# Optimization experiments

Hardware: AMD Instinct MI355X
Metric: run time of the kernel (lower is better)

The kernel has to match this reference:

```python
import jax, jax.numpy as jnp
import numpy as np

D_MODEL = 512; D_K = 64; D_V = 64; H = 8; NX = 6; D_FF = 2048; VOCAB = 37000
BN_EPS = 1e-5


def setup_inputs() -> dict:
    key = jax.random.key(0)
    ks = jax.random.split(key, 20)
    B, S, SE = 4, 512, 512
    g = lambda k, shape, sc: jax.random.normal(k, shape, jnp.float32) * sc
    return {
        'output': jax.random.randint(ks[0], (B, S), 0, VOCAB),
        'encoder_result': g(ks[1], (B, SE, D_MODEL), 1.0),
        'emb': g(ks[2], (VOCAB, D_MODEL), 0.02),
        'Wq1': g(ks[3], (NX, H, D_MODEL, D_K), 0.04),
        'Wk1': g(ks[4], (NX, H, D_MODEL, D_K), 0.04),
        'Wv1': g(ks[5], (NX, H, D_MODEL, D_V), 0.04),
        'Wo1': g(ks[6], (NX, H * D_V, D_MODEL), 0.04),
        'Wq2': g(ks[7], (NX, H, D_MODEL, D_K), 0.04),
        'Wk2': g(ks[8], (NX, H, D_MODEL, D_K), 0.04),
        'Wv2': g(ks[9], (NX, H, D_MODEL, D_V), 0.04),
        'Wo2': g(ks[10], (NX, H * D_V, D_MODEL), 0.04),
        'gamma': jnp.ones((NX, 3, D_MODEL), jnp.float32),
        'beta': jnp.zeros((NX, 3, D_MODEL), jnp.float32),
        'W1': g(ks[11], (NX, D_MODEL, D_FF), 0.04),
        'b1': jnp.zeros((NX, D_FF), jnp.float32),
        'W2': g(ks[12], (NX, D_FF, D_MODEL), 0.02),
        'b2': jnp.zeros((NX, D_MODEL), jnp.float32),
        'Wout': g(ks[13], (D_MODEL, VOCAB), 0.04),
        'bout': jnp.zeros((VOCAB,), jnp.float32),
    }


def _mha(xq, xkv, Wq, Wk, Wv, Wo, causal):
    # Wq/Wk/Wv: [H, D, dk]; batched form of the original per-head Linear loop
    Q = jnp.einsum('bsd,hde->bhse', xq, Wq)
    K = jnp.einsum('btd,hde->bhte', xkv, Wk)
    V = jnp.einsum('btd,hde->bhte', xkv, Wv)
    scores = jnp.einsum('bhse,bhte->bhst', Q, K) / jnp.sqrt(jnp.float32(D_K))
    if causal:
        s = xq.shape[1]
        m = jnp.triu(jnp.ones((s, s), bool), 1)  # future positions
        scores = jnp.where(m, -jnp.inf, scores)
    A = jax.nn.softmax(scores, axis=-1)
    out = jnp.einsum('bhst,bhte->bhse', A, V)  # [B,H,S,dv]
    out = out.transpose(0, 2, 1, 3).reshape(xq.shape[0], xq.shape[1], H * D_V)
    return out @ Wo


def _bn(x, g, b):
    # BatchNorm1d(d_model) in training mode on [B, D, S] == per-channel over (B, S)
    mu = x.mean(axis=(0, 1))
    var = x.var(axis=(0, 1))  # biased, matches torch BN normalization
    return (x - mu) * jax.lax.rsqrt(var + BN_EPS) * g + b


def reference(output, encoder_result, emb, Wq1, Wk1, Wv1, Wo1, Wq2, Wk2, Wv2, Wo2,
              gamma, beta, W1, b1, W2, b2, Wout, bout):
    x = emb[output] * np.sqrt(D_K).astype(np.float32)  # note: sqrt(d_k), as in source
    for i in range(NX):
        x = _bn(x + _mha(x, x, Wq1[i], Wk1[i], Wv1[i], Wo1[i], True), gamma[i, 0], beta[i, 0])
        x = _bn(x + _mha(x, encoder_result, Wq2[i], Wk2[i], Wv2[i], Wo2[i], False), gamma[i, 1], beta[i, 1])
        ff = jax.nn.relu(x @ W1[i] + b1[i]) @ W2[i] + b2[i]
        x = _bn(x + ff, gamma[i, 2], beta[i, 2])
    return jax.nn.softmax(x @ Wout + bout, axis=-1)
```

## Files before the change

kernel.cpp:

```cpp
#include <hip/hip_runtime.h>
#include <math.h>

static constexpr int Bc   = 4;
static constexpr int Sc   = 512;
static constexpr int Dc   = 512;
static constexpr int Hc   = 8;
static constexpr int DKc  = 64;
static constexpr int NXc  = 6;
static constexpr int DFFc = 2048;
static constexpr int Vc   = 37000;
static constexpr int Mc   = Bc * Sc;
static constexpr float BN_EPS = 1e-5f;

#define NEG_INF (-1e30f)

using bf16x8 = __attribute__((ext_vector_type(8))) short;
using f32x4  = __attribute__((ext_vector_type(4))) float;

__device__ inline unsigned short f2bf(float f) {
  union { float f; unsigned u; } v; v.f = f;
  unsigned r = v.u + 0x7FFFu + ((v.u >> 16) & 1u);
  return (unsigned short)(r >> 16);
}

__device__ inline bf16x8 cvt8(float4 a, float4 b) {
  union { bf16x8 v; unsigned short s[8]; } u;
  u.s[0] = f2bf(a.x); u.s[1] = f2bf(a.y); u.s[2] = f2bf(a.z); u.s[3] = f2bf(a.w);
  u.s[4] = f2bf(b.x); u.s[5] = f2bf(b.y); u.s[6] = f2bf(b.z); u.s[7] = f2bf(b.w);
  return u.v;
}

__device__ inline bf16x8 pack8(const float* f) {
  union { bf16x8 v; unsigned short s[8]; } u;
#pragma unroll
  for (int i = 0; i < 8; i++) u.s[i] = f2bf(f[i]);
  return u.v;
}

__global__ void embed_k(const int* __restrict__ idx, const float* __restrict__ emb,
                        float* __restrict__ x) {
  int i = blockIdx.x * blockDim.x + threadIdx.x;
  if (i >= Mc * Dc) return;
  int r = i >> 9;
  int d = i & 511;
  x[i] = emb[(long)idx[r] * Dc + d] * 8.0f;
}

__global__ __launch_bounds__(256) void gemm_nn_mfma(
    const float* __restrict__ A, const float* __restrict__ B0,
    const float* __restrict__ bias, float* __restrict__ C,
    int M, int N, int K, long aB, long bB, long cB,
    float alpha, int relu)
{
  int z = blockIdx.z;
  const float* Ap = A  + (long)z * aB;
  const float* Bp = B0 + (long)z * bB;
  C += (long)z * cB;

  __shared__ unsigned short sA[128 * 32];
  __shared__ unsigned short sB[128 * 32];

  int tid  = threadIdx.x;
  int lane = tid & 63;
  int wave = tid >> 6;
  int row0 = blockIdx.x * 128, col0 = blockIdx.y * 128;

  int ar = tid >> 1, akh = (tid & 1) * 16;
  int bcc = tid & 127, bkh = (tid >> 7) * 16;
  bool bok = (col0 + bcc < N);

  float4 ra[4];
  float  rbs[16];

  auto load_tiles = [&](int k0) {
#pragma unroll
    for (int p = 0; p < 4; p++)
      ra[p] = *(const float4*)(Ap + (long)(row0 + ar) * K + k0 + akh + p * 4);
#pragma unroll
    for (int i = 0; i < 16; i++)
      rbs[i] = bok ? Bp[(long)(k0 + bkh + i) * N + col0 + bcc] : 0.f;
  };

  f32x4 zero4 = {0.f, 0.f, 0.f, 0.f};
  f32x4 acc[4][4];
#pragma unroll
  for (int i = 0; i < 4; i++)
#pragma unroll
    for (int j = 0; j < 4; j++) acc[i][j] = zero4;

  int m0 = (wave >> 1) * 64, n0 = (wave & 1) * 64;
  int fr = lane & 15;

  int aU0 = (ar >> 4) * 64 + ((akh >> 3) + 0) * 16 + (ar & 15);
  int aU1 = (ar >> 4) * 64 + ((akh >> 3) + 1) * 16 + (ar & 15);
  int bU0 = (bcc >> 4) * 64 + ((bkh >> 3) + 0) * 16 + (bcc & 15);
  int bU1 = (bcc >> 4) * 64 + ((bkh >> 3) + 1) * 16 + (bcc & 15);

  load_tiles(0);
  for (int k0 = 0; ; ) {
    __syncthreads();
    *(bf16x8*)&sA[aU0 * 8] = cvt8(ra[0], ra[1]);
    *(bf16x8*)&sA[aU1 * 8] = cvt8(ra[2], ra[3]);
    *(bf16x8*)&sB[bU0 * 8] = pack8(&rbs[0]);
    *(bf16x8*)&sB[bU1 * 8] = pack8(&rbs[8]);
    __syncthreads();

    int kn = k0 + 32;
    bool more = kn < K;
    if (more) load_tiles(kn);

    bf16x8 af[4], bfr[4];
#pragma unroll
    for (int i = 0; i < 4; i++) {
      af[i]  = *(const bf16x8*)&sA[(((m0 >> 4) + i) * 64 + lane) * 8];
      bfr[i] = *(const bf16x8*)&sB[(((n0 >> 4) + i) * 64 + lane) * 8];
    }
#pragma unroll
    for (int mi = 0; mi < 4; mi++)
#pragma unroll
      for (int ni = 0; ni < 4; ni++)
        acc[mi][ni] = __builtin_amdgcn_mfma_f32_16x16x32_bf16(af[mi], bfr[ni], acc[mi][ni], 0, 0, 0);

    if (!more) break;
    k0 = kn;
  }

  int rg = (lane >> 4) << 2;
#pragma unroll
  for (int ni = 0; ni < 4; ni++) {
    int col = col0 + n0 + ni * 16 + fr;
    if (col < N) {
      float bv = bias ? bias[col] : 0.f;
#pragma unroll
      for (int mi = 0; mi < 4; mi++) {
        int r0 = row0 + m0 + mi * 16 + rg;
#pragma unroll
        for (int j = 0; j < 4; j++) {
          float o = acc[mi][ni][j] * alpha + bv;
          if (relu) o = fmaxf(o, 0.f);
          C[(long)(r0 + j) * N + col] = o;
        }
      }
    }
  }
}

__global__ __launch_bounds__(256) void gemm64(
    const float* __restrict__ A, const float* __restrict__ A2,
    const float* __restrict__ B0, const float* __restrict__ B1, const float* __restrict__ B2,
    const float* __restrict__ bias, float* __restrict__ C,
    int N, int K, long aB, long bB, long cB, int mode, int relu)
{
  int z = blockIdx.z;
  const float* Ap;
  const float* Bp;
  float* Cp;
  int ldc;
  if (mode == 2) {
    int t = z >> 5, zz = z & 31;
    Ap = (t == 0 ? A : A2) + (long)(zz >> 3) * aB;
    Bp = (t == 0 ? B0 : (t == 1 ? B1 : B2)) + (long)(zz & 7) * bB;
    Cp = C + (long)z * cB; ldc = N;
  } else if (mode == 3) {
    Ap = A + (long)z * aB; Bp = B0 + (long)z * bB;
    Cp = C + (long)(z >> 3) * ((long)Sc * Dc) + (long)(z & 7) * 64; ldc = Dc;
  } else {
    Ap = A + (long)z * aB; Bp = B0 + (long)z * bB;
    Cp = C + (long)z * cB; ldc = N;
  }

  __shared__ unsigned short sA[64 * 64];
  __shared__ unsigned short sB[64 * 64];

  int tid = threadIdx.x, lane = tid & 63, wave = tid >> 6;
  int row0 = blockIdx.x * 64, col0 = blockIdx.y * 64;

  int ar = tid >> 2, akq = (tid & 3) * 16;
  int bcc = lane, bkq = wave * 16;

  float4 ra[4];
  float  rbs[16];
  auto load_tiles = [&](int k0) {
#pragma unroll
    for (int p = 0; p < 4; p++)
      ra[p] = *(const float4*)(Ap + (long)(row0 + ar) * K + k0 + akq + p * 4);
#pragma unroll
    for (int i = 0; i < 16; i++)
      rbs[i] = Bp[(long)(k0 + bkq + i) * N + col0 + bcc];
  };

  int aU0 = ((ar >> 4) * 2 + (akq >> 5)) * 64 + ((akq >> 3) & 3) * 16 + (ar & 15);
  int aU1 = ((ar >> 4) * 2 + ((akq + 8) >> 5)) * 64 + (((akq + 8) >> 3) & 3) * 16 + (ar & 15);
  int bU0 = ((bcc >> 4) * 2 + (bkq >> 5)) * 64 + ((bkq >> 3) & 3) * 16 + (bcc & 15);
  int bU1 = ((bcc >> 4) * 2 + ((bkq + 8) >> 5)) * 64 + (((bkq + 8) >> 3) & 3) * 16 + (bcc & 15);

  f32x4 zero4 = {0.f, 0.f, 0.f, 0.f};
  f32x4 acc[2][2];
  acc[0][0] = zero4; acc[0][1] = zero4; acc[1][0] = zero4; acc[1][1] = zero4;

  int m0 = (wave >> 1) * 32, n0 = (wave & 1) * 32;
  int fr = lane & 15;

  load_tiles(0);
  for (int k0 = 0; ; ) {
    __syncthreads();
    *(bf16x8*)&sA[aU0 * 8] = cvt8(ra[0], ra[1]);
    *(bf16x8*)&sA[aU1 * 8] = cvt8(ra[2], ra[3]);
    *(bf16x8*)&sB[bU0 * 8] = pack8(&rbs[0]);
    *(bf16x8*)&sB[bU1 * 8] = pack8(&rbs[8]);
    __syncthreads();

    int kn = k0 + 64;
    bool more = kn < K;
    if (more) load_tiles(kn);

    bf16x8 af[2][2], bf[2][2];
#pragma unroll
    for (int i = 0; i < 2; i++)
#pragma unroll
      for (int kk = 0; kk < 2; kk++) {
        af[i][kk] = *(const bf16x8*)&sA[((((m0 >> 4) + i) * 2 + kk) * 64 + lane) * 8];
        bf[i][kk] = *(const bf16x8*)&sB[((((n0 >> 4) + i) * 2 + kk) * 64 + lane) * 8];
      }
#pragma unroll
    for (int kk = 0; kk < 2; kk++)
#pragma unroll
      for (int mi = 0; mi < 2; mi++)
#pragma unroll
        for (int ni = 0; ni < 2; ni++)
          acc[mi][ni] = __builtin_amdgcn_mfma_f32_16x16x32_bf16(af[mi][kk], bf[ni][kk], acc[mi][ni], 0, 0, 0);

    if (!more) break;
    k0 = kn;
  }

  int rg = (lane >> 4) << 2;
#pragma unroll
  for (int ni = 0; ni < 2; ni++) {
    int col = col0 + n0 + ni * 16 + fr;
    float bv = bias ? bias[col] : 0.f;
#pragma unroll
    for (int mi = 0; mi < 2; mi++) {
      int r0 = row0 + m0 + mi * 16 + rg;
#pragma unroll
      for (int j = 0; j < 4; j++) {
        float o = acc[mi][ni][j] + bv;
        if (relu) o = fmaxf(o, 0.f);
        Cp[(long)(r0 + j) * ldc + col] = o;
      }
    }
  }
}

__global__ __launch_bounds__(256) void gemm_nt_mfma(
    const float* __restrict__ A, const float* __restrict__ Bm, float* __restrict__ C,
    long aB, long bB, long cB, float alpha, int causal)
{
  if (causal && blockIdx.y > blockIdx.x) return;
  int z = blockIdx.z;
  const float* Ap = A  + (long)z * aB;
  const float* Bp = Bm + (long)z * bB;
  float* Cp = C + (long)z * cB;

  int tid = threadIdx.x, lane = tid & 63, wave = tid >> 6;
  int m0 = blockIdx.x * 128 + (wave >> 1) * 64;
  int n0 = blockIdx.y * 128 + (wave & 1) * 64;
  int fr = lane & 15, fk = (lane >> 4) * 8;

  bf16x8 af[4][2];
#pragma unroll
  for (int mi = 0; mi < 4; mi++) {
    const float* p = Ap + (long)(m0 + mi * 16 + fr) * DKc + fk;
    af[mi][0] = cvt8(*(const float4*)p,        *(const float4*)(p + 4));
    af[mi][1] = cvt8(*(const float4*)(p + 32), *(const float4*)(p + 36));
  }

  f32x4 zero4 = {0.f, 0.f, 0.f, 0.f};
  f32x4 acc[4][4];
#pragma unroll
  for (int i = 0; i < 4; i++)
#pragma unroll
    for (int j = 0; j < 4; j++) acc[i][j] = zero4;

#pragma unroll
  for (int ni = 0; ni < 4; ni++) {
    const float* q = Bp + (long)(n0 + ni * 16 + fr) * DKc + fk;
    bf16x8 b0 = cvt8(*(const float4*)q,        *(const float4*)(q + 4));
    bf16x8 b1 = cvt8(*(const float4*)(q + 32), *(const float4*)(q + 36));
#pragma unroll
    for (int mi = 0; mi < 4; mi++) {
      acc[mi][ni] = __builtin_amdgcn_mfma_f32_16x16x32_bf16(af[mi][0], b0, acc[mi][ni], 0, 0, 0);
      acc[mi][ni] = __builtin_amdgcn_mfma_f32_16x16x32_bf16(af[mi][1], b1, acc[mi][ni], 0, 0, 0);
    }
  }

  int rg = (lane >> 4) << 2;
#pragma unroll
  for (int ni = 0; ni < 4; ni++) {
    int col = n0 + ni * 16 + fr;
#pragma unroll
    for (int mi = 0; mi < 4; mi++) {
      int r0 = m0 + mi * 16 + rg;
#pragma unroll
      for (int j = 0; j < 4; j++)
        Cp[(long)(r0 + j) * Sc + col] = acc[mi][ni][j] * alpha;
    }
  }
}

__global__ __launch_bounds__(256) void attn_softmax(float* __restrict__ sc, int causal) {
  int row = blockIdx.x;
  int s = row & (Sc - 1);
  float* p = sc + (long)row * Sc;
  int t0 = threadIdx.x, t1 = threadIdx.x + 256;
  int limit = causal ? (s + 1) : Sc;

  float v0 = (t0 < limit) ? p[t0] : NEG_INF;
  float v1 = (t1 < limit) ? p[t1] : NEG_INF;
  float mx = fmaxf(v0, v1);
  __shared__ float sm[4], sm2[4];
#pragma unroll
  for (int o = 32; o > 0; o >>= 1) mx = fmaxf(mx, __shfl_down(mx, o, 64));
  if ((threadIdx.x & 63) == 0) sm[threadIdx.x >> 6] = mx;
  __syncthreads();
  mx = fmaxf(fmaxf(sm[0], sm[1]), fmaxf(sm[2], sm[3]));

  float e0 = (t0 < limit) ? __expf(v0 - mx) : 0.f;
  float e1 = (t1 < limit) ? __expf(v1 - mx) : 0.f;
  float sum = e0 + e1;
#pragma unroll
  for (int o = 32; o > 0; o >>= 1) sum += __shfl_down(sum, o, 64);
  if ((threadIdx.x & 63) == 0) sm2[threadIdx.x >> 6] = sum;
  __syncthreads();
  sum = sm2[0] + sm2[1] + sm2[2] + sm2[3];
  float inv = 1.f / sum;
  p[t0] = e0 * inv;
  p[t1] = e1 * inv;
}

__global__ __launch_bounds__(256) void add_stats(
    float* __restrict__ x, const float* __restrict__ y, float* __restrict__ part)
{
  int blk = blockIdx.x;
  int c = threadIdx.x * 2;
  int r0 = blk * 16;
  float s0 = 0.f, s1 = 0.f, q0 = 0.f, q1 = 0.f;
#pragma unroll 4
  for (int r = r0; r < r0 + 16; r++) {
    long off = (long)r * Dc + c;
    float2 v = *(const float2*)&x[off];
    float2 w = *(const float2*)&y[off];
    v.x += w.x; v.y += w.y;
    *(float2*)&x[off] = v;
    s0 += v.x; q0 += v.x * v.x;
    s1 += v.y; q1 += v.y * v.y;
  }
  part[(long)c * 128 + blk] = s0;
  part[(long)(c + 1) * 128 + blk] = s1;
  part[Dc * 128 + (long)c * 128 + blk] = q0;
  part[Dc * 128 + (long)(c + 1) * 128 + blk] = q1;
}

__global__ __launch_bounds__(256) void bn_finalize(
    const float* __restrict__ part, const float* __restrict__ g,
    const float* __restrict__ b, float* __restrict__ scale, float* __restrict__ shift)
{
  int c = blockIdx.x * 256 + threadIdx.x;
  if (c >= Dc) return;
  const float* ps = part + (long)c * 128;
  const float* pq = part + Dc * 128 + (long)c * 128;
  float s = 0.f, q = 0.f;
#pragma unroll 8
  for (int i = 0; i < 128; i++) { s += ps[i]; q += pq[i]; }
  float mu  = s * (1.f / Mc);
  float var = q * (1.f / Mc) - mu * mu;
  float sc = g[c] * rsqrtf(var + BN_EPS);
  scale[c] = sc;
  shift[c] = b[c] - mu * sc;
}

__global__ void bn_apply(float* __restrict__ x, const float* __restrict__ scale,
                         const float* __restrict__ shift) {
  int i = blockIdx.x * blockDim.x + threadIdx.x;
  if (i >= Mc * Dc) return;
  int c = i & 511;
  x[i] = x[i] * scale[c] + shift[c];
}

static constexpr int VT = 37;
__global__ __launch_bounds__(1024) void vocab_softmax(float* __restrict__ out) {
  long row = blockIdx.x;
  float* p = out + row * (long)Vc;
  float v[VT];
  float mx = NEG_INF;
#pragma unroll
  for (int j = 0; j < VT; j++) {
    int c = threadIdx.x + j * 1024;
    v[j] = (c < Vc) ? p[c] : NEG_INF;
    mx = fmaxf(mx, v[j]);
  }
  __shared__ float sm[16], sm2[16];
#pragma unroll
  for (int o = 32; o > 0; o >>= 1) mx = fmaxf(mx, __shfl_down(mx, o, 64));
  if ((threadIdx.x & 63) == 0) sm[threadIdx.x >> 6] = mx;
  __syncthreads();
  float m2 = sm[0];
#pragma unroll
  for (int i = 1; i < 16; i++) m2 = fmaxf(m2, sm[i]);
  mx = m2;

  float sum = 0.f;
#pragma unroll
  for (int j = 0; j < VT; j++) {
    int c = threadIdx.x + j * 1024;
    float e = (c < Vc) ? __expf(v[j] - mx) : 0.f;
    v[j] = e; sum += e;
  }
#pragma unroll
  for (int o = 32; o > 0; o >>= 1) sum += __shfl_down(sum, o, 64);
  if ((threadIdx.x & 63) == 0) sm2[threadIdx.x >> 6] = sum;
  __syncthreads();
  float s2 = 0.f;
#pragma unroll
  for (int i = 0; i < 16; i++) s2 += sm2[i];
  float inv = 1.f / s2;
#pragma unroll
  for (int j = 0; j < VT; j++) {
    int c = threadIdx.x + j * 1024;
    if (c < Vc) p[c] = v[j] * inv;
  }
}

extern "C" void kernel_launch(void* const* d_in, const int* in_sizes, int n_in,
                              void* d_out, int out_size, void* d_ws, size_t ws_size,
                              hipStream_t stream) {
  const int*   idx   = (const int*)d_in[0];
  const float* enc   = (const float*)d_in[1];
  const float* emb   = (const float*)d_in[2];
  const float* Wq1   = (const float*)d_in[3];
  const float* Wk1   = (const float*)d_in[4];
  const float* Wv1   = (const float*)d_in[5];
  const float* Wo1   = (const float*)d_in[6];
  const float* Wq2   = (const float*)d_in[7];
  const float* Wk2   = (const float*)d_in[8];
  const float* Wv2   = (const float*)d_in[9];
  const float* Wo2   = (const float*)d_in[10];
  const float* gamma = (const float*)d_in[11];
  const float* beta  = (const float*)d_in[12];
  const float* W1    = (const float*)d_in[13];
  const float* b1    = (const float*)d_in[14];
  const float* W2    = (const float*)d_in[15];
  const float* b2    = (const float*)d_in[16];
  const float* Wout  = (const float*)d_in[17];
  const float* bout  = (const float*)d_in[18];
  float* out = (float*)d_out;

  float* ws = (float*)d_ws;
  const long MD = (long)Mc * Dc;
  float* x      = ws;
  float* t0     = x  + MD;
  float* Q      = t0 + MD;
  float* Kb     = Q  + MD;
  float* Vb     = Kb + MD;
  float* cc     = Vb + MD;
  float* ff1    = cc + MD;
  float* scores = ff1 + (long)Mc * DFFc;
  float* scalep = scores + (long)Bc * Hc * Sc * Sc;
  float* shiftp = scalep + Dc;
  float* part   = shiftp + Dc;

  const int n1 = Mc * Dc;
  const int eb = (n1 + 255) / 256;
  const long sSD  = (long)Sc * Dc;
  const long sDK  = (long)Dc * DKc;
  const long sSK  = (long)Sc * DKc;
  const long sSS  = (long)Sc * Sc;

  embed_k<<<eb, 256, 0, stream>>>(idx, emb, x);

  for (int l = 0; l < NXc; l++) {
    {
      const float* wq = Wq1 + (long)l * Hc * Dc * DKc;
      const float* wk = Wk1 + (long)l * Hc * Dc * DKc;
      const float* wv = Wv1 + (long)l * Hc * Dc * DKc;
      const float* wo = Wo1 + (long)l * Dc * Dc;
      gemm64<<<dim3(Sc / 64, 1, 96), 256, 0, stream>>>(
          x, x, wq, wk, wv, nullptr, Q, DKc, Dc, sSD, sDK, sSK, 2, 0);
      gemm_nt_mfma<<<dim3(4, 4, Bc * Hc), 256, 0, stream>>>(
          Q, Kb, scores, sSK, sSK, sSS, 0.125f, 1);
      attn_softmax<<<Bc * Hc * Sc, 256, 0, stream>>>(scores, 1);
      gemm64<<<dim3(Sc / 64, 1, Bc * Hc), 256, 0, stream>>>(
          scores, nullptr, Vb, nullptr, nullptr, nullptr, cc, DKc, Sc, sSS, sSK, 0, 3, 0);
      gemm64<<<dim3(Mc / 64, Dc / 64, 1), 256, 0, stream>>>(
          cc, nullptr, wo, nullptr, nullptr, nullptr, t0, Dc, Dc, 0, 0, 0, 0, 0);
      add_stats<<<128, 256, 0, stream>>>(x, t0, part);
      bn_finalize<<<2, 256, 0, stream>>>(part, gamma + (long)(l * 3 + 0) * Dc, beta + (long)(l * 3 + 0) * Dc, scalep, shiftp);
      bn_apply<<<eb, 256, 0, stream>>>(x, scalep, shiftp);
    }
    {
      const float* wq = Wq2 + (long)l * Hc * Dc * DKc;
      const float* wk = Wk2 + (long)l * Hc * Dc * DKc;
      const float* wv = Wv2 + (long)l * Hc * Dc * DKc;
      const float* wo = Wo2 + (long)l * Dc * Dc;
      gemm64<<<dim3(Sc / 64, 1, 96), 256, 0, stream>>>(
          x, enc, wq, wk, wv, nullptr, Q, DKc, Dc, sSD, sDK, sSK, 2, 0);
      gemm_nt_mfma<<<dim3(4, 4, Bc * Hc), 256, 0, stream>>>(
          Q, Kb, scores, sSK, sSK, sSS, 0.125f, 0);
      attn_softmax<<<Bc * Hc * Sc, 256, 0, stream>>>(scores, 0);
      gemm64<<<dim3(Sc / 64, 1, Bc * Hc), 256, 0, stream>>>(
          scores, nullptr, Vb, nullptr, nullptr, nullptr, cc, DKc, Sc, sSS, sSK, 0, 3, 0);
      gemm64<<<dim3(Mc / 64, Dc / 64, 1), 256, 0, stream>>>(
          cc, nullptr, wo, nullptr, nullptr, nullptr, t0, Dc, Dc, 0, 0, 0, 0, 0);
      add_stats<<<128, 256, 0, stream>>>(x, t0, part);
      bn_finalize<<<2, 256, 0, stream>>>(part, gamma + (long)(l * 3 + 1) * Dc, beta + (long)(l * 3 + 1) * Dc, scalep, shiftp);
      bn_apply<<<eb, 256, 0, stream>>>(x, scalep, shiftp);
    }
    {
      gemm_nn_mfma<<<dim3(Mc / 128, DFFc / 128, 1), 256, 0, stream>>>(
          x, W1 + (long)l * Dc * DFFc, b1 + (long)l * DFFc, ff1,
          Mc, DFFc, Dc, 0, 0, 0, 1.f, 1);
      gemm64<<<dim3(Mc / 64, Dc / 64, 1), 256, 0, stream>>>(
          ff1, nullptr, W2 + (long)l * DFFc * Dc, nullptr, nullptr, b2 + (long)l * Dc, t0,
          Dc, DFFc, 0, 0, 0, 0, 0);
      add_stats<<<128, 256, 0, stream>>>(x, t0, part);
      bn_finalize<<<2, 256, 0, stream>>>(part, gamma + (long)(l * 3 + 2) * Dc, beta + (long)(l * 3 + 2) * Dc, scalep, shiftp);
      bn_apply<<<eb, 256, 0, stream>>>(x, scalep, shiftp);
    }
  }

  gemm_nn_mfma<<<dim3(Mc / 128, (Vc + 127) / 128, 1), 256, 0, stream>>>(
      x, Wout, bout, out, Mc, Vc, Dc, 0, 0, 0, 1.f, 0);
  vocab_softmax<<<Mc, 1024, 0, stream>>>(out);
}
```

Before: 2.420 ms.

## Convert activations and weights to bf16 with transposed layouts and direct-to-LDS loads

Adds a weight conversion kernel that transposes all projection, FFN and output weights into bf16 K-major layouts, either all up front or per layer depending on workspace size. Activations (x, encoder output, Q/K/V, attention probabilities, FFN hidden) are now stored as bf16 alongside fp32 x. The GEMMs are rewritten to load bf16 tiles straight into LDS with global_load_lds, and the large GEMMs use a 128x128 kernel with an LDS-staged, vectorised epilogue. The aim is less global memory traffic and no in-kernel fp32-to-bf16 conversion, at the price of an extra weight-conversion pass on every call and lower precision of stored intermediates.

```diff
diff --git a/kernel.cpp b/kernel.cpp
--- a/kernel.cpp
+++ b/kernel.cpp
@@ -14,252 +14,300 @@
 
 #define NEG_INF (-1e30f)
 
+typedef unsigned short u16;
 using bf16x8 = __attribute__((ext_vector_type(8))) short;
+using us8    = __attribute__((ext_vector_type(8))) unsigned short;
 using f32x4  = __attribute__((ext_vector_type(4))) float;
 
-__device__ inline unsigned short f2bf(float f) {
+__device__ inline u16 f2bf(float f) {
   union { float f; unsigned u; } v; v.f = f;
   unsigned r = v.u + 0x7FFFu + ((v.u >> 16) & 1u);
-  return (unsigned short)(r >> 16);
-}
-
-__device__ inline bf16x8 cvt8(float4 a, float4 b) {
-  union { bf16x8 v; unsigned short s[8]; } u;
-  u.s[0] = f2bf(a.x); u.s[1] = f2bf(a.y); u.s[2] = f2bf(a.z); u.s[3] = f2bf(a.w);
-  u.s[4] = f2bf(b.x); u.s[5] = f2bf(b.y); u.s[6] = f2bf(b.z); u.s[7] = f2bf(b.w);
-  return u.v;
-}
-
-__device__ inline bf16x8 pack8(const float* f) {
-  union { bf16x8 v; unsigned short s[8]; } u;
-#pragma unroll
-  for (int i = 0; i < 8; i++) u.s[i] = f2bf(f[i]);
-  return u.v;
+  return (u16)(r >> 16);
+}
+
+__device__ inline void gload16(const void* g, void* l) {
+  __builtin_amdgcn_global_load_lds(
+      (const __attribute__((address_space(1))) unsigned int*)g,
+      (__attribute__((address_space(3))) unsigned int*)l, 16, 0, 0);
 }
 
 __global__ void embed_k(const int* __restrict__ idx, const float* __restrict__ emb,
-                        float* __restrict__ x) {
+                        float* __restrict__ x, u16* __restrict__ xh) {
   int i = blockIdx.x * blockDim.x + threadIdx.x;
   if (i >= Mc * Dc) return;
-  int r = i >> 9;
-  int d = i & 511;
-  x[i] = emb[(long)idx[r] * Dc + d] * 8.0f;
-}
-
-__global__ __launch_bounds__(256) void gemm_nn_mfma(
-    const float* __restrict__ A, const float* __restrict__ B0,
-    const float* __restrict__ bias, float* __restrict__ C,
-    int M, int N, int K, long aB, long bB, long cB,
-    float alpha, int relu)
+  int r = i >> 9, d = i & 511;
+  float v = emb[(long)idx[r] * Dc + d] * 8.0f;
+  x[i] = v;
+  xh[i] = f2bf(v);
+}
+
+__global__ void cvt_bf16(const float* __restrict__ in, u16* __restrict__ out, int n4) {
+  int i = blockIdx.x * blockDim.x + threadIdx.x;
+  if (i >= n4) return;
+  float4 v = ((const float4*)in)[i];
+  unsigned a = (unsigned)f2bf(v.x) | ((unsigned)f2bf(v.y) << 16);
+  unsigned b = (unsigned)f2bf(v.z) | ((unsigned)f2bf(v.w) << 16);
+  uint2 w; w.x = a; w.y = b;
+  ((uint2*)out)[i] = w;
+}
+
+__device__ void wtile(const float* src, int ldin, int cval, u16* dst, int ldout) {
+  __shared__ u16 ls[64][65];
+  int tx = threadIdx.x & 63, ty = threadIdx.x >> 6;
+#pragma unroll
+  for (int p = 0; p < 16; p++) {
+    int r = p * 4 + ty;
+    float v = (tx < cval) ? src[(long)r * ldin + tx] : 0.f;
+    ls[tx][r] = f2bf(v);
+  }
+  __syncthreads();
+#pragma unroll
+  for (int p = 0; p < 16; p++) {
+    int oc = p * 4 + ty;
+    dst[(long)oc * ldout + tx] = ls[oc][tx];
+  }
+}
+
+__global__ __launch_bounds__(256) void wconv(
+    const float* q1, const float* k1, const float* v1, const float* o1,
+    const float* q2, const float* k2, const float* v2, const float* o2,
+    const float* w1, const float* w2, const float* wout,
+    u16* Wb, u16* WoutT, int nl, int l0)
 {
-  int z = blockIdx.z;
-  const float* Ap = A  + (long)z * aB;
-  const float* Bp = B0 + (long)z * bB;
-  C += (long)z * cB;
-
-  __shared__ unsigned short sA[128 * 32];
-  __shared__ unsigned short sB[128 * 32];
-
-  int tid  = threadIdx.x;
-  int lane = tid & 63;
-  int wave = tid >> 6;
+  long HT = (long)nl * 262144;
+  int u = blockIdx.x;
+  int layerBlocks = nl * 1024;
+  if (u < layerBlocks) {
+    int lslot = u >> 10;
+    int l = l0 + lslot;
+    int t = u & 1023;
+    if (t < 384) {
+      int ten = t >> 6, w = t & 63, h = w >> 3, rt = w & 7;
+      const float* base = (ten == 0) ? q1 : (ten == 1) ? k1 : (ten == 2) ? v1
+                         : (ten == 3) ? q2 : (ten == 4) ? k2 : v2;
+      const float* src = base + ((long)l * 8 + h) * 32768 + (long)rt * 64 * 64;
+      u16* dst = Wb + (long)ten * HT + (long)lslot * 262144 + (long)h * 32768 + rt * 64;
+      wtile(src, 64, 64, dst, 512);
+    } else if (t < 512) {
+      int v_ = t - 384, o = v_ >> 6, w = v_ & 63, rt = w >> 3, ct = w & 7;
+      const float* src = (o ? o2 : o1) + (long)l * 262144 + (long)rt * 64 * 512 + ct * 64;
+      u16* dst = Wb + (long)(6 + o) * HT + (long)lslot * 262144 + (long)ct * 64 * 512 + rt * 64;
+      wtile(src, 512, 64, dst, 512);
+    } else if (t < 768) {
+      int v_ = t - 512, rt = v_ >> 5, ct = v_ & 31;
+      const float* src = w1 + (long)l * 1048576 + (long)rt * 64 * 2048 + ct * 64;
+      u16* dst = Wb + 8 * HT + (long)lslot * 1048576 + (long)ct * 64 * 512 + rt * 64;
+      wtile(src, 2048, 64, dst, 512);
+    } else {
+      int v_ = t - 768, rt = v_ >> 3, ct = v_ & 7;
+      const float* src = w2 + (long)l * 1048576 + (long)rt * 64 * 512 + ct * 64;
+      u16* dst = Wb + 12 * HT + (long)lslot * 1048576 + (long)ct * 64 * 2048 + rt * 64;
+      wtile(src, 512, 64, dst, 2048);
+    }
+  } else {
+    int v_ = u - layerBlocks;
+    int rt = v_ & 7, ct = v_ >> 3;
+    int c0 = ct * 64;
+    int cv = Vc - c0; cv = cv < 0 ? 0 : (cv > 64 ? 64 : cv);
+    const float* src = wout + (long)rt * 64 * Vc + c0;
+    u16* dst = WoutT + (long)c0 * 512 + rt * 64;
+    wtile(src, Vc, cv, dst, 512);
+  }
+}
+
+__global__ __launch_bounds__(256) void gemm128(
+    const u16* __restrict__ A, const u16* __restrict__ Bt,
+    const float* __restrict__ bias, void* __restrict__ Cv,
+    int N, int K, int obf, int relu)
+{
+  __shared__ u16 smem[2 * 128 * 64];
+  u16* sA = smem;
+  u16* sB = smem + 128 * 64;
+
+  int tid = threadIdx.x, lane = tid & 63, wave = tid >> 6;
   int row0 = blockIdx.x * 128, col0 = blockIdx.y * 128;
-
-  int ar = tid >> 1, akh = (tid & 1) * 16;
-  int bcc = tid & 127, bkh = (tid >> 7) * 16;
-  bool bok = (col0 + bcc < N);
-
-  float4 ra[4];
-  float  rbs[16];
-
-  auto load_tiles = [&](int k0) {
-#pragma unroll
-    for (int p = 0; p < 4; p++)
-      ra[p] = *(const float4*)(Ap + (long)(row0 + ar) * K + k0 + akh + p * 4);
-#pragma unroll
-    for (int i = 0; i < 16; i++)
-      rbs[i] = bok ? Bp[(long)(k0 + bkh + i) * N + col0 + bcc] : 0.f;
-  };
-
-  f32x4 zero4 = {0.f, 0.f, 0.f, 0.f};
+  int frs = lane & 15, kq = lane >> 4;
+
+  const u16* pA[4]; const u16* pB[4]; u16* lA[4]; u16* lB[4];
+#pragma unroll
+  for (int i = 0; i < 4; i++) {
+    int idx = wave * 4 + i, mi = idx >> 1, kgh = idx & 1;
+    pA[i] = A  + (long)(row0 + mi * 16 + frs) * K + kgh * 32 + kq * 8;
+    pB[i] = Bt + (long)(col0 + mi * 16 + frs) * K + kgh * 32 + kq * 8;
+    lA[i] = sA + (mi * 2 + kgh) * 512;
+    lB[i] = sB + (mi * 2 + kgh) * 512;
+  }
+
   f32x4 acc[4][4];
 #pragma unroll
   for (int i = 0; i < 4; i++)
 #pragma unroll
-    for (int j = 0; j < 4; j++) acc[i][j] = zero4;
+    for (int j = 0; j < 4; j++) acc[i][j] = (f32x4){0.f, 0.f, 0.f, 0.f};
 
   int m0 = (wave >> 1) * 64, n0 = (wave & 1) * 64;
-  int fr = lane & 15;
-
-  int aU0 = (ar >> 4) * 64 + ((akh >> 3) + 0) * 16 + (ar & 15);
-  int aU1 = (ar >> 4) * 64 + ((akh >> 3) + 1) * 16 + (ar & 15);
-  int bU0 = (bcc >> 4) * 64 + ((bkh >> 3) + 0) * 16 + (bcc & 15);
-  int bU1 = (bcc >> 4) * 64 + ((bkh >> 3) + 1) * 16 + (bcc & 15);
-
-  load_tiles(0);
-  for (int k0 = 0; ; ) {
+
+  for (int kt = 0; kt < K; kt += 64) {
+#pragma unroll
+    for (int i = 0; i < 4; i++) { gload16(pA[i], lA[i]); pA[i] += 64; }
+#pragma unroll
+    for (int i = 0; i < 4; i++) { gload16(pB[i], lB[i]); pB[i] += 64; }
     __syncthreads();
-    *(bf16x8*)&sA[aU0 * 8] = cvt8(ra[0], ra[1]);
-    *(bf16x8*)&sA[aU1 * 8] = cvt8(ra[2], ra[3]);
-    *(bf16x8*)&sB[bU0 * 8] = pack8(&rbs[0]);
-    *(bf16x8*)&sB[bU1 * 8] = pack8(&rbs[8]);
+#pragma unroll
+    for (int ks = 0; ks < 2; ks++) {
+      bf16x8 af[4], bf[4];
+#pragma unroll
+      for (int i = 0; i < 4; i++) {
+        af[i] = *(const bf16x8*)&sA[(((m0 >> 4) + i) * 128 + ks * 64 + lane) * 8];
+        bf[i] = *(const bf16x8*)&sB[(((n0 >> 4) + i) * 128 + ks * 64 + lane) * 8];
+      }
+#pragma unroll
+      for (int mi = 0; mi < 4; mi++)
+#pragma unroll
+        for (int ni = 0; ni < 4; ni++)
+          acc[mi][ni] = __builtin_amdgcn_mfma_f32_16x16x32_bf16(af[mi], bf[ni], acc[mi][ni], 0, 0, 0);
+    }
     __syncthreads();
-
-    int kn = k0 + 32;
-    bool more = kn < K;
-    if (more) load_tiles(kn);
-
-    bf16x8 af[4], bfr[4];
-#pragma unroll
-    for (int i = 0; i < 4; i++) {
-      af[i]  = *(const bf16x8*)&sA[(((m0 >> 4) + i) * 64 + lane) * 8];
-      bfr[i] = *(const bf16x8*)&sB[(((n0 >> 4) + i) * 64 + lane) * 8];
-    }
-#pragma unroll
-    for (int mi = 0; mi < 4; mi++)
-#pragma unroll
-      for (int ni = 0; ni < 4; ni++)
-        acc[mi][ni] = __builtin_amdgcn_mfma_f32_16x16x32_bf16(af[mi], bfr[ni], acc[mi][ni], 0, 0, 0);
-
-    if (!more) break;
-    k0 = kn;
-  }
-
-  int rg = (lane >> 4) << 2;
-#pragma unroll
-  for (int ni = 0; ni < 4; ni++) {
-    int col = col0 + n0 + ni * 16 + fr;
-    if (col < N) {
-      float bv = bias ? bias[col] : 0.f;
-#pragma unroll
-      for (int mi = 0; mi < 4; mi++) {
-        int r0 = row0 + m0 + mi * 16 + rg;
-#pragma unroll
-        for (int j = 0; j < 4; j++) {
-          float o = acc[mi][ni][j] * alpha + bv;
-          if (relu) o = fmaxf(o, 0.f);
-          C[(long)(r0 + j) * N + col] = o;
-        }
-      }
-    }
-  }
-}
-
-__global__ __launch_bounds__(256) void gemm64(
-    const float* __restrict__ A, const float* __restrict__ A2,
-    const float* __restrict__ B0, const float* __restrict__ B1, const float* __restrict__ B2,
-    const float* __restrict__ bias, float* __restrict__ C,
-    int N, int K, long aB, long bB, long cB, int mode, int relu)
-{
-  int z = blockIdx.z;
-  const float* Ap;
-  const float* Bp;
-  float* Cp;
-  int ldc;
-  if (mode == 2) {
-    int t = z >> 5, zz = z & 31;
-    Ap = (t == 0 ? A : A2) + (long)(zz >> 3) * aB;
-    Bp = (t == 0 ? B0 : (t == 1 ? B1 : B2)) + (long)(zz & 7) * bB;
-    Cp = C + (long)z * cB; ldc = N;
-  } else if (mode == 3) {
-    Ap = A + (long)z * aB; Bp = B0 + (long)z * bB;
-    Cp = C + (long)(z >> 3) * ((long)Sc * Dc) + (long)(z & 7) * 64; ldc = Dc;
-  } else {
-    Ap = A + (long)z * aB; Bp = B0 + (long)z * bB;
-    Cp = C + (long)z * cB; ldc = N;
-  }
-
-  __shared__ unsigned short sA[64 * 64];
-  __shared__ unsigned short sB[64 * 64];
-
-  int tid = threadIdx.x, lane = tid & 63, wave = tid >> 6;
-  int row0 = blockIdx.x * 64, col0 = blockIdx.y * 64;
-
-  int ar = tid >> 2, akq = (tid & 3) * 16;
-  int bcc = lane, bkq = wave * 16;
-
-  float4 ra[4];
-  float  rbs[16];
-  auto load_tiles = [&](int k0) {
-#pragma unroll
-    for (int p = 0; p < 4; p++)
-      ra[p] = *(const float4*)(Ap + (long)(row0 + ar) * K + k0 + akq + p * 4);
-#pragma unroll
-    for (int i = 0; i < 16; i++)
-      rbs[i] = Bp[(long)(k0 + bkq + i) * N + col0 + bcc];
-  };
-
-  int aU0 = ((ar >> 4) * 2 + (akq >> 5)) * 64 + ((akq >> 3) & 3) * 16 + (ar & 15);
-  int aU1 = ((ar >> 4) * 2 + ((akq + 8) >> 5)) * 64 + (((akq + 8) >> 3) & 3) * 16 + (ar & 15);
-  int bU0 = ((bcc >> 4) * 2 + (bkq >> 5)) * 64 + ((bkq >> 3) & 3) * 16 + (bcc & 15);
-  int bU1 = ((bcc >> 4) * 2 + ((bkq + 8) >> 5)) * 64 + (((bkq + 8) >> 3) & 3) * 16 + (bcc & 15);
-
-  f32x4 zero4 = {0.f, 0.f, 0.f, 0.f};
-  f32x4 acc[2][2];
-  acc[0][0] = zero4; acc[0][1] = zero4; acc[1][0] = zero4; acc[1][1] = zero4;
-
-  int m0 = (wave >> 1) * 32, n0 = (wave & 1) * 32;
-  int fr = lane & 15;
-
-  load_tiles(0);
-  for (int k0 = 0; ; ) {
-    __syncthreads();
-    *(bf16x8*)&sA[aU0 * 8] = cvt8(ra[0], ra[1]);
-    *(bf16x8*)&sA[aU1 * 8] = cvt8(ra[2], ra[3]);
-    *(bf16x8*)&sB[bU0 * 8] = pack8(&rbs[0]);
-    *(bf16x8*)&sB[bU1 * 8] = pack8(&rbs[8]);
-    __syncthreads();
-
-    int kn = k0 + 64;
-    bool more = kn < K;
-    if (more) load_tiles(kn);
-
-    bf16x8 af[2][2], bf[2][2];
-#pragma unroll
-    for (int i = 0; i < 2; i++)
-#pragma unroll
-      for (int kk = 0; kk < 2; kk++) {
-        af[i][kk] = *(const bf16x8*)&sA[((((m0 >> 4) + i) * 2 + kk) * 64 + lane) * 8];
-        bf[i][kk] = *(const bf16x8*)&sB[((((n0 >> 4) + i) * 2 + kk) * 64 + lane) * 8];
-      }
-#pragma unroll
-    for (int kk = 0; kk < 2; kk++)
-#pragma unroll
-      for (int mi = 0; mi < 2; mi++)
-#pragma unroll
-        for (int ni = 0; ni < 2; ni++)
-          acc[mi][ni] = __builtin_amdgcn_mfma_f32_16x16x32_bf16(af[mi][kk], bf[ni][kk], acc[mi][ni], 0, 0, 0);
-
-    if (!more) break;
-    k0 = kn;
-  }
-
-  int rg = (lane >> 4) << 2;
-#pragma unroll
-  for (int ni = 0; ni < 2; ni++) {
-    int col = col0 + n0 + ni * 16 + fr;
-    float bv = bias ? bias[col] : 0.f;
-#pragma unroll
-    for (int mi = 0; mi < 2; mi++) {
-      int r0 = row0 + m0 + mi * 16 + rg;
+  }
+
+  float* scr = (float*)smem + wave * (16 * 68);
+  int rg = kq * 4;
+  u16* Cus = (u16*)Cv; float* Cf = (float*)Cv;
+#pragma unroll
+  for (int mi = 0; mi < 4; mi++) {
+#pragma unroll
+    for (int ni = 0; ni < 4; ni++) {
+      int colg = col0 + n0 + ni * 16 + frs;
+      float bv = bias ? ((colg < N) ? bias[colg] : 0.f) : 0.f;
 #pragma unroll
       for (int j = 0; j < 4; j++) {
         float o = acc[mi][ni][j] + bv;
         if (relu) o = fmaxf(o, 0.f);
-        Cp[(long)(r0 + j) * ldc + col] = o;
+        scr[(rg + j) * 68 + ni * 16 + frs] = o;
       }
     }
+    int rbase = row0 + m0 + mi * 16;
+    if (obf) {
+#pragma unroll
+      for (int p = 0; p < 2; p++) {
+        int rowl = p * 8 + (lane >> 3), c8 = (lane & 7) * 8;
+        float4 v0 = *(const float4*)&scr[rowl * 68 + c8];
+        float4 v1 = *(const float4*)&scr[rowl * 68 + c8 + 4];
+        union { us8 v; u16 s[8]; } w;
+        w.s[0] = f2bf(v0.x); w.s[1] = f2bf(v0.y); w.s[2] = f2bf(v0.z); w.s[3] = f2bf(v0.w);
+        w.s[4] = f2bf(v1.x); w.s[5] = f2bf(v1.y); w.s[6] = f2bf(v1.z); w.s[7] = f2bf(v1.w);
+        *(us8*)&Cus[(long)(rbase + rowl) * N + col0 + n0 + c8] = w.v;
+      }
+    } else {
+#pragma unroll
+      for (int p = 0; p < 4; p++) {
+        int rowl = p * 4 + kq, c4 = frs * 4;
+        int colg = col0 + n0 + c4;
+        float4 v = *(const float4*)&scr[rowl * 68 + c4];
+        if (colg < N)
+          *(float4*)&Cf[(long)(rbase + rowl) * N + colg] = v;
+      }
+    }
+  }
+}
+
+__global__ __launch_bounds__(256) void gemm64(
+    const u16* __restrict__ A, const u16* __restrict__ A2,
+    const u16* __restrict__ Bt, const float* __restrict__ bias, void* __restrict__ Cv,
+    int N, int K, int lda, long aB, long btB, long cB, long tQK, int mode, int obf)
+{
+  int z = blockIdx.z;
+  const u16* Ap; const u16* Btp; long coff; int ldc;
+  if (mode == 1) {
+    int t = z >> 5, zz = z & 31;
+    Ap = (t == 0 ? A : A2) + (long)(zz >> 3) * aB;
+    Btp = Bt + (long)t * tQK + (long)(zz & 7) * btB;
+    coff = (long)z * cB; ldc = N;
+  } else if (mode == 2) {
+    Ap = A + (long)(z & 7) * aB;
+    Btp = Bt + (long)(z >> 3) * btB;
+    coff = (long)z * cB; ldc = N;
+  } else if (mode == 3) {
+    Ap = A + (long)z * aB;
+    Btp = Bt + (long)z * btB;
+    coff = (long)(z >> 3) * (512 * 512) + (long)(z & 7) * 64; ldc = 512;
+  } else {
+    Ap = A + (long)z * aB;
+    Btp = Bt + (long)z * btB;
+    coff = (long)z * cB; ldc = N;
+  }
+
+  __shared__ u16 smem[2 * 64 * 64];
+  u16* sA = smem; u16* sB = smem + 4096;
+
+  int tid = threadIdx.x, lane = tid & 63, wave = tid >> 6;
+  int row0 = blockIdx.x * 64, col0 = blockIdx.y * 64;
+  int frs = lane & 15, kq = lane >> 4;
+
+  const u16* pA[2]; const u16* pB[2]; u16* lA[2]; u16* lB[2];
+#pragma unroll
+  for (int i = 0; i < 2; i++) {
+    pA[i] = Ap  + (long)(row0 + wave * 16 + frs) * lda + i * 32 + kq * 8;
+    pB[i] = Btp + (long)(col0 + wave * 16 + frs) * K   + i * 32 + kq * 8;
+    lA[i] = sA + (wave * 2 + i) * 512;
+    lB[i] = sB + (wave * 2 + i) * 512;
+  }
+
+  f32x4 acc[2][2];
+  acc[0][0] = acc[0][1] = acc[1][0] = acc[1][1] = (f32x4){0.f, 0.f, 0.f, 0.f};
+  int m0 = (wave >> 1) * 32, n0 = (wave & 1) * 32;
+
+  for (int kt = 0; kt < K; kt += 64) {
+#pragma unroll
+    for (int i = 0; i < 2; i++) {
+      gload16(pA[i], lA[i]); pA[i] += 64;
+      gload16(pB[i], lB[i]); pB[i] += 64;
+    }
+    __syncthreads();
+    bf16x8 af[2][2], bf[2][2];
+#pragma unroll
+    for (int i = 0; i < 2; i++)
+#pragma unroll
+      for (int ks = 0; ks < 2; ks++) {
+        af[i][ks] = *(const bf16x8*)&sA[(((m0 >> 4) + i) * 128 + ks * 64 + lane) * 8];
+        bf[i][ks] = *(const bf16x8*)&sB[(((n0 >> 4) + i) * 128 + ks * 64 + lane) * 8];
+      }
+#pragma unroll
+    for (int ks = 0; ks < 2; ks++)
+#pragma unroll
+      for (int mi = 0; mi < 2; mi++)
+#pragma unroll
+        for (int ni = 0; ni < 2; ni++)
+          acc[mi][ni] = __builtin_amdgcn_mfma_f32_16x16x32_bf16(af[mi][ks], bf[ni][ks], acc[mi][ni], 0, 0, 0);
+    __syncthreads();
+  }
+
+  int rg = kq * 4;
+  u16* Cus = (u16*)Cv + coff; float* Cf = (float*)Cv + coff;
+#pragma unroll
+  for (int ni = 0; ni < 2; ni++) {
+    int col = col0 + n0 + ni * 16 + frs;
+    float bv = bias ? bias[col] : 0.f;
+#pragma unroll
+    for (int mi = 0; mi < 2; mi++) {
+      int r0 = row0 + m0 + mi * 16 + rg;
+#pragma unroll
+      for (int j = 0; j < 4; j++) {
+        float o = acc[mi][ni][j] + bv;
+        if (obf) Cus[(long)(r0 + j) * ldc + col] = f2bf(o);
+        else     Cf [(long)(r0 + j) * ldc + col] = o;
+      }
+    }
   }
 }
 
 __global__ __launch_bounds__(256) void gemm_nt_mfma(
-    const float* __restrict__ A, const float* __restrict__ Bm, float* __restrict__ C,
+    const u16* __restrict__ A, const u16* __restrict__ Bm, float* __restrict__ C,
     long aB, long bB, long cB, float alpha, int causal)
 {
   if (causal && blockIdx.y > blockIdx.x) return;
   int z = blockIdx.z;
-  const float* Ap = A  + (long)z * aB;
-  const float* Bp = Bm + (long)z * bB;
+  const u16* Ap = A + (long)z * aB;
+  const u16* Bp = Bm + (long)z * bB;
   float* Cp = C + (long)z * cB;
 
   int tid = threadIdx.x, lane = tid & 63, wave = tid >> 6;
@@ -270,23 +318,22 @@
   bf16x8 af[4][2];
 #pragma unroll
   for (int mi = 0; mi < 4; mi++) {
-    const float* p = Ap + (long)(m0 + mi * 16 + fr) * DKc + fk;
-    af[mi][0] = cvt8(*(const float4*)p,        *(const float4*)(p + 4));
-    af[mi][1] = cvt8(*(const float4*)(p + 32), *(const float4*)(p + 36));
-  }
-
-  f32x4 zero4 = {0.f, 0.f, 0.f, 0.f};
+    const u16* p = Ap + (long)(m0 + mi * 16 + fr) * DKc + fk;
+    af[mi][0] = *(const bf16x8*)p;
+    af[mi][1] = *(const bf16x8*)(p + 32);
+  }
+
   f32x4 acc[4][4];
 #pragma unroll
   for (int i = 0; i < 4; i++)
 #pragma unroll
-    for (int j = 0; j < 4; j++) acc[i][j] = zero4;
+    for (int j = 0; j < 4; j++) acc[i][j] = (f32x4){0.f, 0.f, 0.f, 0.f};
 
 #pragma unroll
   for (int ni = 0; ni < 4; ni++) {
-    const float* q = Bp + (long)(n0 + ni * 16 + fr) * DKc + fk;
-    bf16x8 b0 = cvt8(*(const float4*)q,        *(const float4*)(q + 4));
-    bf16x8 b1 = cvt8(*(const float4*)(q + 32), *(const float4*)(q + 36));
+    const u16* q = Bp + (long)(n0 + ni * 16 + fr) * DKc + fk;
+    bf16x8 b0 = *(const bf16x8*)q;
+    bf16x8 b1 = *(const bf16x8*)(q + 32);
 #pragma unroll
     for (int mi = 0; mi < 4; mi++) {
       acc[mi][ni] = __builtin_amdgcn_mfma_f32_16x16x32_bf16(af[mi][0], b0, acc[mi][ni], 0, 0, 0);
@@ -312,6 +359,7 @@
   int row = blockIdx.x;
   int s = row & (Sc - 1);
   float* p = sc + (long)row * Sc;
+  u16* pb = (u16*)p;
   int t0 = threadIdx.x, t1 = threadIdx.x + 256;
   int limit = causal ? (s + 1) : Sc;
 
@@ -334,8 +382,8 @@
   __syncthreads();
   sum = sm2[0] + sm2[1] + sm2[2] + sm2[3];
   float inv = 1.f / sum;
-  p[t0] = e0 * inv;
-  p[t1] = e1 * inv;
+  pb[t0] = f2bf(e0 * inv);
+  pb[t1] = f2bf(e1 * inv);
 }
 
 __global__ __launch_bounds__(256) void add_stats(
@@ -379,12 +427,14 @@
   shift[c] = b[c] - mu * sc;
 }
 
-__global__ void bn_apply(float* __restrict__ x, const float* __restrict__ scale,
-                         const float* __restrict__ shift) {
+__global__ void bn_apply(float* __restrict__ x, u16* __restrict__ xh,
+                         const float* __restrict__ scale, const float* __restrict__ shift) {
   int i = blockIdx.x * blockDim.x + threadIdx.x;
   if (i >= Mc * Dc) return;
   int c = i & 511;
-  x[i] = x[i] * scale[c] + shift[c];
+  float v = x[i] * scale[c] + shift[c];
+  x[i] = v;
+  xh[i] = f2bf(v);
 }
 
 static constexpr int VT = 37;
@@ -456,79 +506,92 @@
   float* out = (float*)d_out;
 
   float* ws = (float*)d_ws;
-  const long MD = (long)Mc * Dc;
-  float* x      = ws;
-  float* t0     = x  + MD;
-  float* Q      = t0 + MD;
-  float* Kb     = Q  + MD;
-  float* Vb     = Kb + MD;
-  float* cc     = Vb + MD;
-  float* ff1    = cc + MD;
-  float* scores = ff1 + (long)Mc * DFFc;
-  float* scalep = scores + (long)Bc * Hc * Sc * Sc;
-  float* shiftp = scalep + Dc;
-  float* part   = shiftp + Dc;
+  size_t off = 0;
+  float* x      = ws + off; off += 1048576;
+  float* t0     = ws + off; off += 1048576;
+  u16*   xh     = (u16*)(ws + off); off += 524288;
+  u16*   Q      = (u16*)(ws + off); off += 524288;
+  u16*   Kb     = (u16*)(ws + off); off += 524288;
+  u16*   Vt     = (u16*)(ws + off); off += 524288;
+  u16*   cc     = (u16*)(ws + off); off += 524288;
+  u16*   ench   = (u16*)(ws + off); off += 524288;
+  float* part   = ws + off; off += 131072;
+  float* scalep = ws + off; off += 512;
+  float* shiftp = ws + off; off += 512;
+  float* scores = ws + off; off += 8388608;
+  u16*   Wb     = (u16*)(ws + off);
+
+  const bool upfront = ws_size >= (off + 22085632 + 8192) * 4;
+  const long HTe = (long)(upfront ? 6 : 1) * 262144;
+  u16* WoutT = upfront ? (Wb + 16 * HTe) : (u16*)scores;
+  u16* ff1h  = (u16*)scores;
 
   const int n1 = Mc * Dc;
   const int eb = (n1 + 255) / 256;
-  const long sSD  = (long)Sc * Dc;
-  const long sDK  = (long)Dc * DKc;
-  const long sSK  = (long)Sc * DKc;
-  const long sSS  = (long)Sc * Sc;
-
-  embed_k<<<eb, 256, 0, stream>>>(idx, emb, x);
+
+  cvt_bf16<<<1024, 256, 0, stream>>>(enc, ench, 262144);
+  if (upfront)
+    wconv<<<6 * 1024 + 4640, 256, 0, stream>>>(Wq1, Wk1, Wv1, Wo1, Wq2, Wk2, Wv2, Wo2,
+                                               W1, W2, Wout, Wb, WoutT, 6, 0);
+  embed_k<<<eb, 256, 0, stream>>>(idx, emb, x, xh);
 
   for (int l = 0; l < NXc; l++) {
+    if (!upfront)
+      wconv<<<1024, 256, 0, stream>>>(Wq1, Wk1, Wv1, Wo1, Wq2, Wk2, Wv2, Wo2,
+                                      W1, W2, Wout, Wb, WoutT, 1, l);
+    const long lsl = upfront ? (long)l : 0;
+    const u16* WqT1l = Wb + 0 * HTe + lsl * 262144;
+    const u16* WvT1l = Wb + 2 * HTe + lsl * 262144;
+    const u16* WqT2l = Wb + 3 * HTe + lsl * 262144;
+    const u16* WvT2l = Wb + 5 * HTe + lsl * 262144;
+    const u16* WoT1l = Wb + 6 * HTe + lsl * 262144;
+    const u16* WoT2l = Wb + 7 * HTe + lsl * 262144;
+    const u16* W1Tl  = Wb + 8 * HTe + lsl * 1048576;
+    const u16* W2Tl  = Wb + 12 * HTe + lsl * 1048576;
+
     {
-      const float* wq = Wq1 + (long)l * Hc * Dc * DKc;
-      const float* wk = Wk1 + (long)l * Hc * Dc * DKc;
-      const float* wv = Wv1 + (long)l * Hc * Dc * DKc;
-      const float* wo = Wo1 + (long)l * Dc * Dc;
-      gemm64<<<dim3(Sc / 64, 1, 96), 256, 0, stream>>>(
-          x, x, wq, wk, wv, nullptr, Q, DKc, Dc, sSD, sDK, sSK, 2, 0);
-      gemm_nt_mfma<<<dim3(4, 4, Bc * Hc), 256, 0, stream>>>(
-          Q, Kb, scores, sSK, sSK, sSS, 0.125f, 1);
+      gemm64<<<dim3(8, 1, 64), 256, 0, stream>>>(
+          xh, xh, WqT1l, nullptr, Q, 64, 512, 512, 262144, 32768, 32768, HTe, 1, 1);
+      gemm64<<<dim3(1, 8, 32), 256, 0, stream>>>(
+          WvT1l, nullptr, xh, nullptr, Vt, 512, 512, 512, 32768, 262144, 32768, 0, 2, 1);
+      gemm_nt_mfma<<<dim3(4, 4, 32), 256, 0, stream>>>(Q, Kb, scores, 32768, 32768, 262144, 0.125f, 1);
       attn_softmax<<<Bc * Hc * Sc, 256, 0, stream>>>(scores, 1);
-      gemm64<<<dim3(Sc / 64, 1, Bc * Hc), 256, 0, stream>>>(
-          scores, nullptr, Vb, nullptr, nullptr, nullptr, cc, DKc, Sc, sSS, sSK, 0, 3, 0);
-      gemm64<<<dim3(Mc / 64, Dc / 64, 1), 256, 0, stream>>>(
-          cc, nullptr, wo, nullptr, nullptr, nullptr, t0, Dc, Dc, 0, 0, 0, 0, 0);
+      gemm64<<<dim3(8, 1, 32), 256, 0, stream>>>(
+          (u16*)scores, nullptr, Vt, nullptr, cc, 64, 512, 1024, 524288, 32768, 0, 0, 3, 1);
+      gemm64<<<dim3(32, 8, 1), 256, 0, stream>>>(
+          cc, nullptr, WoT1l, nullptr, t0, 512, 512, 512, 0, 0, 0, 0, 0, 0);
       add_stats<<<128, 256, 0, stream>>>(x, t0, part);
       bn_finalize<<<2, 256, 0, stream>>>(part, gamma + (long)(l * 3 + 0) * Dc, beta + (long)(l * 3 + 0) * Dc, scalep, shiftp);
-      bn_apply<<<eb, 256, 0, stream>>>(x, scalep, shiftp);
+      bn_apply<<<eb, 256, 0, stream>>>(x, xh, scalep, shiftp);
     }
     {
-      const float* wq = Wq2 + (long)l * Hc * Dc * DKc;
-      const float* wk = Wk2 + (long)l * Hc * Dc * DKc;
-      const float* wv = Wv2 + (long)l * Hc * Dc * DKc;
-      const float* wo = Wo2 + (long)l * Dc * Dc;
-      gemm64<<<dim3(Sc / 64, 1, 96), 256, 0, stream>>>(
-          x, enc, wq, wk, wv, nullptr, Q, DKc, Dc, sSD, sDK, sSK, 2, 0);
-      gemm_nt_mfma<<<dim3(4, 4, Bc * Hc), 256, 0, stream>>>(
-          Q, Kb, scores, sSK, sSK, sSS, 0.125f, 0);
+      gemm64<<<dim3(8, 1, 64), 256, 0, stream>>>(
+          xh, ench, WqT2l, nullptr, Q, 64, 512, 512, 262144, 32768, 32768, HTe, 1, 1);
+      gemm64<<<dim3(1, 8, 32), 256, 0, stream>>>(
+          WvT2l, nullptr, ench, nullptr, Vt, 512, 512, 512, 32768, 262144, 32768, 0, 2, 1);
+      gemm_nt_mfma<<<dim3(4, 4, 32), 256, 0, stream>>>(Q, Kb, scores, 32768, 32768, 262144, 0.125f, 0);
       attn_softmax<<<Bc * Hc * Sc, 256, 0, stream>>>(scores, 0);
-      gemm64<<<dim3(Sc / 64, 1, Bc * Hc), 256, 0, stream>>>(
-          scores, nullptr, Vb, nullptr, nullptr, nullptr, cc, DKc, Sc, sSS, sSK, 0, 3, 0);
-      gemm64<<<dim3(Mc / 64, Dc / 64, 1), 256, 0, stream>>>(
-          cc, nullptr, wo, nullptr, nullptr, nullptr, t0, Dc, Dc, 0, 0, 0, 0, 0);
+      gemm64<<<dim3(8, 1, 32), 256, 0, stream>>>(
+          (u16*)scores, nullptr, Vt, nullptr, cc, 64, 512, 1024, 524288, 32768, 0, 0, 3, 1);
+      gemm64<<<dim3(32, 8, 1), 256, 0, stream>>>(
+          cc, nullptr, WoT2l, nullptr, t0, 512, 512, 512, 0, 0, 0, 0, 0, 0);
       add_stats<<<128, 256, 0, stream>>>(x, t0, part);
       bn_finalize<<<2, 256, 0, stream>>>(part, gamma + (long)(l * 3 + 1) * Dc, beta + (long)(l * 3 + 1) * Dc, scalep, shiftp);
-      bn_apply<<<eb, 256, 0, stream>>>(x, scalep, shiftp);
+      bn_apply<<<eb, 256, 0, stream>>>(x, xh, scalep, shiftp);
     }
     {
-      gemm_nn_mfma<<<dim3(Mc / 128, DFFc / 128, 1), 256, 0, stream>>>(
-          x, W1 + (long)l * Dc * DFFc, b1 + (long)l * DFFc, ff1,
-          Mc, DFFc, Dc, 0, 0, 0, 1.f, 1);
-      gemm64<<<dim3(Mc / 64, Dc / 64, 1), 256, 0, stream>>>(
-          ff1, nullptr, W2 + (long)l * DFFc * Dc, nullptr, nullptr, b2 + (long)l * Dc, t0,
-          Dc, DFFc, 0, 0, 0, 0, 0);
+      gemm128<<<dim3(16, 16), 256, 0, stream>>>(xh, W1Tl, b1 + (long)l * DFFc, ff1h, 2048, 512, 1, 1);
+      gemm64<<<dim3(32, 8, 1), 256, 0, stream>>>(
+          ff1h, nullptr, W2Tl, b2 + (long)l * Dc, t0, 512, 2048, 2048, 0, 0, 0, 0, 0, 0);
       add_stats<<<128, 256, 0, stream>>>(x, t0, part);
       bn_finalize<<<2, 256, 0, stream>>>(part, gamma + (long)(l * 3 + 2) * Dc, beta + (long)(l * 3 + 2) * Dc, scalep, shiftp);
-      bn_apply<<<eb, 256, 0, stream>>>(x, scalep, shiftp);
-    }
-  }
-
-  gemm_nn_mfma<<<dim3(Mc / 128, (Vc + 127) / 128, 1), 256, 0, stream>>>(
-      x, Wout, bout, out, Mc, Vc, Dc, 0, 0, 0, 1.f, 0);
+      bn_apply<<<eb, 256, 0, stream>>>(x, xh, scalep, shiftp);
+    }
+  }
+
+  if (!upfront)
+    wconv<<<4640, 256, 0, stream>>>(Wq1, Wk1, Wv1, Wo1, Wq2, Wk2, Wv2, Wo2,
+                                    W1, W2, Wout, Wb, WoutT, 0, 0);
+  gemm128<<<dim3(16, 290), 256, 0, stream>>>(xh, WoutT, bout, out, Vc, 512, 0, 0);
   vocab_softmax<<<Mc, 1024, 0, stream>>>(out);
 }
```

New measurement: 2.325 ms. 1.04x faster.
